# Optimization experiments

Measured on AMD Instinct MI355X. Metric: run time of the kernel, lower is better.

## Reference

```python
import jax, jax.numpy as jnp
import numpy as np

S = 30.0   # scale
M = 0.3    # additive angular margin (arcface)
EPS = 1e-07


def setup_inputs() -> dict:
    key = jax.random.key(0)
    k1, k2, k3 = jax.random.split(key, 3)
    N, D, C = 8192, 256, 10000
    x = jax.random.normal(k1, (N, D), dtype=jnp.float32)
    W = jax.random.normal(k2, (C, D), dtype=jnp.float32) * 0.05  # linear weight [C, D]
    target = jax.random.randint(k3, (N,), 0, C)
    return {"x": x, "W": W, "target": target}


def reference(x, W, target):
    # L2-normalize inputs along features. NOTE: the torch code's loop that
    # 'normalizes' weight_fc params is a no-op (rebinds a local), so W is
    # intentionally NOT normalized here, matching the original math.
    xn = x / jnp.linalg.norm(x, axis=1, keepdims=True)
    logits = xn @ W.T                                   # [N, C]
    n = logits.shape[0]
    tgt = logits[jnp.arange(n), target]                 # [N] target-class cosine-like score
    # arcface margin: s * cos(acos(clamp(t)) + m)
    numerator = S * jnp.cos(jnp.arccos(jnp.clip(tgt, -1.0 + EPS, 1.0 - EPS)) + M)
    # exclude-target sum: sum_j exp(s*logits) minus the target column (no [N,C-1] concat)
    exp_s = jnp.exp(S * logits)                         # [N, C]
    sum_excl = jnp.sum(exp_s, axis=1) - jnp.exp(S * tgt)
    denominator = jnp.exp(numerator) + sum_excl
    L = numerator - jnp.log(denominator)
    return -jnp.mean(L)
```

## Files before the change

kernel.cpp:

```cpp
#include <hip/hip_runtime.h>
#include <hip/hip_bf16.h>
#include <stdint.h>

#define S_SCALE 30.0f
#define S_L2E_SC 0.33813165020835f
#define N_ROWS 8192
#define D_DIM 256
#define C_CLS 10000
#define NCB 8

typedef __attribute__((ext_vector_type(4))) float f32x4;

static __device__ __forceinline__ void gl16(const void* g, void* l) {
  __builtin_amdgcn_global_load_lds(
      (const __attribute__((address_space(1))) void*)g,
      (__attribute__((address_space(3))) void*)l, 16, 0, 0);
}

static __device__ __forceinline__ long u2l(uint2 v) {
  union { uint2 u; long l; } x; x.u = v; return x.l;
}

static __device__ __forceinline__ float row_sum16(float v) {
  union { float f; int i; } u, w;
  u.f = v;
  w.i = __builtin_amdgcn_update_dpp(0, u.i, 0xB1, 0xF, 0xF, true);  u.f += w.f;
  w.i = __builtin_amdgcn_update_dpp(0, u.i, 0x4E, 0xF, 0xF, true);  u.f += w.f;
  w.i = __builtin_amdgcn_update_dpp(0, u.i, 0x141, 0xF, 0xF, true); u.f += w.f;
  w.i = __builtin_amdgcn_update_dpp(0, u.i, 0x140, 0xF, 0xF, true); u.f += w.f;
  return u.f;
}

__global__ __launch_bounds__(256) void k_prep(const float* __restrict__ x,
                                              const float* __restrict__ W,
                                              const int* __restrict__ target,
                                              unsigned char* __restrict__ xnb8,
                                              unsigned char* __restrict__ WbF8,
                                              float* __restrict__ tgt) {
  if (blockIdx.x < 1280) {
    int gidx = blockIdx.x * 256 + threadIdx.x;
    int lane = gidx & 63;
    int kc = (gidx >> 6) & 7;
    int c16 = gidx >> 9;
    int col = c16 * 16 + (lane & 15);
    int k0 = kc * 32 + (lane >> 4) * 8;
    int r0 = 0, r1 = 0;
    if (col < C_CLS) {
      const float4 a = *(const float4*)(W + (size_t)col * D_DIM + k0);
      const float4 b = *(const float4*)(W + (size_t)col * D_DIM + k0 + 4);
      r0 = __builtin_amdgcn_cvt_pk_fp8_f32(a.x * 16.f, a.y * 16.f, 0, false);
      r0 = __builtin_amdgcn_cvt_pk_fp8_f32(a.z * 16.f, a.w * 16.f, r0, true);
      r1 = __builtin_amdgcn_cvt_pk_fp8_f32(b.x * 16.f, b.y * 16.f, 0, false);
      r1 = __builtin_amdgcn_cvt_pk_fp8_f32(b.z * 16.f, b.w * 16.f, r1, true);
    }
    size_t dst = (size_t)(c16 >> 1) * 8192 + (size_t)kc * 1024 +
                 (size_t)lane * 16 + (size_t)(c16 & 1) * 8;
    *(int2*)(WbF8 + dst) = (int2){r0, r1};
  } else {
    int row = (blockIdx.x - 1280) * 4 + (threadIdx.x >> 6);
    int l = threadIdx.x & 63;
    const float4 v = *(const float4*)(x + (size_t)row * D_DIM + l * 4);
    float ss = v.x * v.x + v.y * v.y + v.z * v.z + v.w * v.w;
#pragma unroll
    for (int m = 1; m < 64; m <<= 1) ss += __shfl_xor(ss, m, 64);
    float rn = 1.0f / sqrtf(ss);
    float s8 = rn * 8.f;
    int r0 = __builtin_amdgcn_cvt_pk_fp8_f32(v.x * s8, v.y * s8, 0, false);
    r0 = __builtin_amdgcn_cvt_pk_fp8_f32(v.z * s8, v.w * s8, r0, true);
    int panel = row >> 7, r16 = (row >> 4) & 7, lr = row & 15;
    size_t dst = (size_t)panel * 32768 + (size_t)(r16 * 8 + (l >> 3)) * 512 +
                 (size_t)(((l >> 1) & 3) * 16 + lr) * 8 + (l & 1) * 4;
    *(int*)(xnb8 + dst) = r0;
    int tc = target[row];
    const float4 b = *(const float4*)(W + (size_t)tc * D_DIM + l * 4);
    float s = v.x * b.x + v.y * b.y + v.z * b.z + v.w * b.w;
#pragma unroll
    for (int m = 1; m < 64; m <<= 1) s += __shfl_xor(s, m, 64);
    if (l == 0) tgt[row] = s * rn;
  }
}

__global__ __launch_bounds__(512, 4) void k_gemm(const unsigned char* __restrict__ xnb8,
                                                 const unsigned char* __restrict__ WbF8,
                                                 float* __restrict__ partials) {
  __shared__ __align__(16) char lds[34816];
  const int b = blockIdx.x;
  const int cg = b & 7;
  const int br = b >> 3;
  const int bc0 = cg * 5;
  const int t = threadIdx.x;
  const int w = t >> 6, l = t & 63;
  const int wr = w >> 2, wc = w & 3;
  const int lr = l & 15, lk = l >> 4;
  float* rsumAll = (float*)(lds + 32768);

  if (t < 512) rsumAll[t] = 0.f;

  {
    const char* Ag = (const char*)xnb8 + (size_t)br * 32768;
#pragma unroll
    for (int i = 0; i < 4; ++i)
      gl16(Ag + i * 8192 + w * 1024 + l * 16, lds + i * 8192 + w * 1024);
    asm volatile("s_waitcnt vmcnt(0)" ::: "memory");
    __builtin_amdgcn_sched_barrier(0);
    __builtin_amdgcn_s_barrier();
  }

  f32x4 acc[4][4];
#pragma unroll
  for (int m = 0; m < 4; m++)
#pragma unroll
    for (int n = 0; n < 4; n++) acc[m][n] = (f32x4){0.f, 0.f, 0.f, 0.f};

  const char* AwL = lds + (size_t)(wr * 4 * 8) * 512 + (size_t)l * 8;
  const unsigned char* Bwv = WbF8 + (size_t)(bc0 * 8 + wc * 2) * 8192 + (size_t)l * 16;
  float* rw = rsumAll + w * 64;

  const int tt0 = w % 5;
  uint4 b0[2], b1[2];
  {
    const unsigned char* Bt = Bwv + (size_t)tt0 * 65536;
    b0[0] = *(const uint4*)(Bt);
    b0[1] = *(const uint4*)(Bt + 8192);
  }

  for (int s = 0; s < 5; ++s) {
    int tt = tt0 + s; if (tt >= 5) tt -= 5;
    int ttn = tt + 1; if (ttn >= 5) ttn -= 5;
    const unsigned char* Bt = Bwv + (size_t)tt * 65536;
    const unsigned char* Btn = Bwv + (size_t)ttn * 65536;

    auto step = [&](int kc, uint4(&cur)[2], uint4(&nxt)[2]) {
      if (kc < 7) {
        nxt[0] = *(const uint4*)(Bt + (kc + 1) * 1024);
        nxt[1] = *(const uint4*)(Bt + 8192 + (kc + 1) * 1024);
      } else if (s < 4) {
        nxt[0] = *(const uint4*)(Btn);
        nxt[1] = *(const uint4*)(Btn + 8192);
      }
      __builtin_amdgcn_s_setprio(1);
#pragma unroll
      for (int fm = 0; fm < 4; ++fm) {
        long a = u2l(*(const uint2*)(AwL + (fm * 8 + kc) * 512));
        acc[fm][0] = __builtin_amdgcn_mfma_f32_16x16x32_fp8_fp8(
            a, u2l((uint2){cur[0].x, cur[0].y}), acc[fm][0], 0, 0, 0);
        acc[fm][1] = __builtin_amdgcn_mfma_f32_16x16x32_fp8_fp8(
            a, u2l((uint2){cur[0].z, cur[0].w}), acc[fm][1], 0, 0, 0);
        acc[fm][2] = __builtin_amdgcn_mfma_f32_16x16x32_fp8_fp8(
            a, u2l((uint2){cur[1].x, cur[1].y}), acc[fm][2], 0, 0, 0);
        acc[fm][3] = __builtin_amdgcn_mfma_f32_16x16x32_fp8_fp8(
            a, u2l((uint2){cur[1].z, cur[1].w}), acc[fm][3], 0, 0, 0);
      }
      __builtin_amdgcn_s_setprio(0);
    };
    step(0, b0, b1); step(1, b1, b0); step(2, b0, b1); step(3, b1, b0);
    step(4, b0, b1); step(5, b1, b0); step(6, b0, b1); step(7, b1, b0);

#pragma unroll
    for (int m = 0; m < 4; ++m) {
      float rs0 = 0.f, rs1 = 0.f, rs2 = 0.f, rs3 = 0.f;
#pragma unroll
      for (int n = 0; n < 4; ++n) {
        rs0 += __builtin_amdgcn_exp2f(acc[m][n][0] * S_L2E_SC);
        rs1 += __builtin_amdgcn_exp2f(acc[m][n][1] * S_L2E_SC);
        rs2 += __builtin_amdgcn_exp2f(acc[m][n][2] * S_L2E_SC);
        rs3 += __builtin_amdgcn_exp2f(acc[m][n][3] * S_L2E_SC);
        acc[m][n] = (f32x4){0.f, 0.f, 0.f, 0.f};
      }
      rs0 = row_sum16(rs0); rs1 = row_sum16(rs1);
      rs2 = row_sum16(rs2); rs3 = row_sum16(rs3);
      if (lr == 0) {
        int row = m * 16 + lk * 4;
        rw[row + 0] += rs0; rw[row + 1] += rs1;
        rw[row + 2] += rs2; rw[row + 3] += rs3;
      }
    }
  }

  __syncthreads();
  if (t < 128) {
    int wr2 = t >> 6, r = t & 63;
    float sv = rsumAll[(wr2 * 4 + 0) * 64 + r] + rsumAll[(wr2 * 4 + 1) * 64 + r] +
               rsumAll[(wr2 * 4 + 2) * 64 + r] + rsumAll[(wr2 * 4 + 3) * 64 + r];
    partials[(size_t)cg * N_ROWS + (size_t)br * 128 + t] = sv;
  }
}

__global__ __launch_bounds__(256) void k_loss1(const float* __restrict__ partials,
                                               const float* __restrict__ tgt,
                                               float* __restrict__ bsum) {
  __shared__ float wsum[4];
  int i = blockIdx.x * 256 + threadIdx.x;
  const float* p = partials + i;
  float s = -240.0f;
#pragma unroll
  for (int j = 0; j < NCB; ++j) s += p[(size_t)j * N_ROWS];
  float tl = tgt[i];
  float tcv = fminf(fmaxf(tl, -1.0f + 1e-7f), 1.0f - 1e-7f);
  const float cm = 0.95533648912560601964f;
  const float sm = 0.29552020666133957510f;
  float num = S_SCALE * (tcv * cm - sqrtf(fmaxf(1.0f - tcv * tcv, 0.f)) * sm);
  float sum_excl = s - __expf(S_SCALE * tl);
  float denom = __expf(num) + sum_excl;
  float L = num - __logf(denom);
#pragma unroll
  for (int m = 1; m < 64; m <<= 1) L += __shfl_xor(L, m, 64);
  int l = threadIdx.x & 63, w = threadIdx.x >> 6;
  if (l == 0) wsum[w] = L;
  __syncthreads();
  if (threadIdx.x == 0) bsum[blockIdx.x] = wsum[0] + wsum[1] + wsum[2] + wsum[3];
}

__global__ void k_loss2(const float* __restrict__ bsum, float* __restrict__ out) {
  float s = 0.f;
  for (int i = 0; i < 32; ++i) s += bsum[i];
  out[0] = -s / (float)N_ROWS;
}

extern "C" void kernel_launch(void* const* d_in, const int* in_sizes, int n_in,
                              void* d_out, int out_size, void* d_ws, size_t ws_size,
                              hipStream_t stream) {
  const float* x = (const float*)d_in[0];
  const float* W = (const float*)d_in[1];
  const int* target = (const int*)d_in[2];
  float* out = (float*)d_out;
  char* ws = (char*)d_ws;

  unsigned char* xnb8 = (unsigned char*)(ws);
  unsigned char* WbF8 = (unsigned char*)(ws + 2097152);
  float* tgt = (float*)(ws + 4718592);
  float* partials = (float*)(ws + 4751360);
  float* bsum = (float*)(ws + 5013504);

  k_prep<<<3328, 256, 0, stream>>>(x, W, target, xnb8, WbF8, tgt);
  k_gemm<<<512, 512, 0, stream>>>(xnb8, WbF8, partials);
  k_loss1<<<32, 256, 0, stream>>>(partials, tgt, bsum);
  k_loss2<<<1, 1, 0, stream>>>(bsum, out);
}
```

Before: 50.25 us.

## Split GEMM blocks into 256-thread halves and deepen B-operand register prefetch

The fused GEMM+exp-sum kernel now launches 1024 blocks of 256 threads, where each pair of blocks splits a column group in half (2x2 waves instead of 2x4), and the partial-sum count doubles to 16. The B-fragment register prefetch goes from double buffering to a 4-slot rotation issued three k-steps ahead, and the per-wave rotated tile start order is dropped. The intent is finer-grained scheduling and better hiding of global-load latency. The cost is loading the A panel into LDS twice as often, more partials to reduce, and more registers per thread.

After: 51.98 us. 3.4% more time.

```diff
diff --git a/kernel.cpp b/kernel.cpp
--- a/kernel.cpp
+++ b/kernel.cpp
@@ -7,7 +7,7 @@
 #define N_ROWS 8192
 #define D_DIM 256
 #define C_CLS 10000
-#define NCB 8
+#define NCB 16
 
 typedef __attribute__((ext_vector_type(4))) float f32x4;
 
@@ -80,27 +80,27 @@
   }
 }
 
-__global__ __launch_bounds__(512, 4) void k_gemm(const unsigned char* __restrict__ xnb8,
+__global__ __launch_bounds__(256, 3) void k_gemm(const unsigned char* __restrict__ xnb8,
                                                  const unsigned char* __restrict__ WbF8,
                                                  float* __restrict__ partials) {
-  __shared__ __align__(16) char lds[34816];
+  __shared__ __align__(16) char lds[33792];
   const int b = blockIdx.x;
   const int cg = b & 7;
-  const int br = b >> 3;
-  const int bc0 = cg * 5;
+  const int sub = (b >> 3) & 1;
+  const int br = b >> 4;
   const int t = threadIdx.x;
   const int w = t >> 6, l = t & 63;
-  const int wr = w >> 2, wc = w & 3;
+  const int wr = w >> 1, wc = w & 1;
   const int lr = l & 15, lk = l >> 4;
   float* rsumAll = (float*)(lds + 32768);
 
-  if (t < 512) rsumAll[t] = 0.f;
+  rsumAll[t] = 0.f;
 
   {
     const char* Ag = (const char*)xnb8 + (size_t)br * 32768;
 #pragma unroll
-    for (int i = 0; i < 4; ++i)
-      gl16(Ag + i * 8192 + w * 1024 + l * 16, lds + i * 8192 + w * 1024);
+    for (int i = 0; i < 8; ++i)
+      gl16(Ag + i * 4096 + w * 1024 + l * 16, lds + i * 4096 + w * 1024);
     asm volatile("s_waitcnt vmcnt(0)" ::: "memory");
     __builtin_amdgcn_sched_barrier(0);
     __builtin_amdgcn_s_barrier();
@@ -113,48 +113,51 @@
     for (int n = 0; n < 4; n++) acc[m][n] = (f32x4){0.f, 0.f, 0.f, 0.f};
 
   const char* AwL = lds + (size_t)(wr * 4 * 8) * 512 + (size_t)l * 8;
-  const unsigned char* Bwv = WbF8 + (size_t)(bc0 * 8 + wc * 2) * 8192 + (size_t)l * 16;
+  const unsigned char* Bwv = WbF8 + (size_t)(cg * 40 + sub * 20 + wc * 2) * 8192 +
+                             (size_t)l * 16;
   float* rw = rsumAll + w * 64;
 
-  const int tt0 = w % 5;
-  uint4 b0[2], b1[2];
-  {
-    const unsigned char* Bt = Bwv + (size_t)tt0 * 65536;
-    b0[0] = *(const uint4*)(Bt);
-    b0[1] = *(const uint4*)(Bt + 8192);
-  }
+  uint4 pA0, pA1, pB0, pB1, pC0, pC1, pD0, pD1;
+  pA0 = *(const uint4*)(Bwv);          pA1 = *(const uint4*)(Bwv + 8192);
+  pB0 = *(const uint4*)(Bwv + 1024);   pB1 = *(const uint4*)(Bwv + 8192 + 1024);
+  pC0 = *(const uint4*)(Bwv + 2048);   pC1 = *(const uint4*)(Bwv + 8192 + 2048);
 
   for (int s = 0; s < 5; ++s) {
-    int tt = tt0 + s; if (tt >= 5) tt -= 5;
-    int ttn = tt + 1; if (ttn >= 5) ttn -= 5;
-    const unsigned char* Bt = Bwv + (size_t)tt * 65536;
-    const unsigned char* Btn = Bwv + (size_t)ttn * 65536;
-
-    auto step = [&](int kc, uint4(&cur)[2], uint4(&nxt)[2]) {
-      if (kc < 7) {
-        nxt[0] = *(const uint4*)(Bt + (kc + 1) * 1024);
-        nxt[1] = *(const uint4*)(Bt + 8192 + (kc + 1) * 1024);
+    const unsigned char* Bt = Bwv + (size_t)s * 32768;
+    const unsigned char* Btn = Bt + 32768;
+
+    auto step = [&](int kc, uint4& c0, uint4& c1, uint4& p0, uint4& p1) {
+      int kcp = kc + 3;
+      if (kcp < 8) {
+        p0 = *(const uint4*)(Bt + kcp * 1024);
+        p1 = *(const uint4*)(Bt + 8192 + kcp * 1024);
       } else if (s < 4) {
-        nxt[0] = *(const uint4*)(Btn);
-        nxt[1] = *(const uint4*)(Btn + 8192);
+        p0 = *(const uint4*)(Btn + (kcp - 8) * 1024);
+        p1 = *(const uint4*)(Btn + 8192 + (kcp - 8) * 1024);
       }
       __builtin_amdgcn_s_setprio(1);
 #pragma unroll
       for (int fm = 0; fm < 4; ++fm) {
         long a = u2l(*(const uint2*)(AwL + (fm * 8 + kc) * 512));
         acc[fm][0] = __builtin_amdgcn_mfma_f32_16x16x32_fp8_fp8(
-            a, u2l((uint2){cur[0].x, cur[0].y}), acc[fm][0], 0, 0, 0);
+            a, u2l((uint2){c0.x, c0.y}), acc[fm][0], 0, 0, 0);
         acc[fm][1] = __builtin_amdgcn_mfma_f32_16x16x32_fp8_fp8(
-            a, u2l((uint2){cur[0].z, cur[0].w}), acc[fm][1], 0, 0, 0);
+            a, u2l((uint2){c0.z, c0.w}), acc[fm][1], 0, 0, 0);
         acc[fm][2] = __builtin_amdgcn_mfma_f32_16x16x32_fp8_fp8(
-            a, u2l((uint2){cur[1].x, cur[1].y}), acc[fm][2], 0, 0, 0);
+            a, u2l((uint2){c1.x, c1.y}), acc[fm][2], 0, 0, 0);
         acc[fm][3] = __builtin_amdgcn_mfma_f32_16x16x32_fp8_fp8(
-            a, u2l((uint2){cur[1].z, cur[1].w}), acc[fm][3], 0, 0, 0);
+            a, u2l((uint2){c1.z, c1.w}), acc[fm][3], 0, 0, 0);
       }
       __builtin_amdgcn_s_setprio(0);
     };
-    step(0, b0, b1); step(1, b1, b0); step(2, b0, b1); step(3, b1, b0);
-    step(4, b0, b1); step(5, b1, b0); step(6, b0, b1); step(7, b1, b0);
+    step(0, pA0, pA1, pD0, pD1);
+    step(1, pB0, pB1, pA0, pA1);
+    step(2, pC0, pC1, pB0, pB1);
+    step(3, pD0, pD1, pC0, pC1);
+    step(4, pA0, pA1, pD0, pD1);
+    step(5, pB0, pB1, pA0, pA1);
+    step(6, pC0, pC1, pB0, pB1);
+    step(7, pD0, pD1, pC0, pC1);
 
 #pragma unroll
     for (int m = 0; m < 4; ++m) {
@@ -180,9 +183,8 @@
   __syncthreads();
   if (t < 128) {
     int wr2 = t >> 6, r = t & 63;
-    float sv = rsumAll[(wr2 * 4 + 0) * 64 + r] + rsumAll[(wr2 * 4 + 1) * 64 + r] +
-               rsumAll[(wr2 * 4 + 2) * 64 + r] + rsumAll[(wr2 * 4 + 3) * 64 + r];
-    partials[(size_t)cg * N_ROWS + (size_t)br * 128 + t] = sv;
+    float sv = rsumAll[(wr2 * 2 + 0) * 64 + r] + rsumAll[(wr2 * 2 + 1) * 64 + r];
+    partials[(size_t)(cg * 2 + sub) * N_ROWS + (size_t)br * 128 + t] = sv;
   }
 }
 
@@ -230,10 +232,10 @@
   unsigned char* WbF8 = (unsigned char*)(ws + 2097152);
   float* tgt = (float*)(ws + 4718592);
   float* partials = (float*)(ws + 4751360);
-  float* bsum = (float*)(ws + 5013504);
+  float* bsum = (float*)(ws + 5275648);
 
   k_prep<<<3328, 256, 0, stream>>>(x, W, target, xnb8, WbF8, tgt);
-  k_gemm<<<512, 512, 0, stream>>>(xnb8, WbF8, partials);
+  k_gemm<<<1024, 256, 0, stream>>>(xnb8, WbF8, partials);
   k_loss1<<<32, 256, 0, stream>>>(partials, tgt, bsum);
   k_loss2<<<1, 1, 0, stream>>>(bsum, out);
 }
```
